# Kernel optimization log

Hardware: AMD Instinct MI355X
Metric: run time of the kernel (lower is better)

Reference implementation:

```python
import jax, jax.numpy as jnp
import numpy as np

B, S, D, H = 8, 4096, 1024, 16
HD = D // H          # 64 head dim
NR = HD // 2         # 32 rotations
BASE = 10000.0


def setup_inputs() -> dict:
    key = jax.random.key(0)
    k0, k1, k2 = jax.random.split(key, 3)
    x = jax.random.normal(k0, (B, S, D), jnp.float32)
    thetas = jax.random.normal(k1, (NR,), jnp.float32) * 0.1
    r_pairs = jax.random.uniform(k2, (NR, 2), jnp.float32) * HD  # float indices in [0, HD)
    theta_scale = jnp.ones((1,), jnp.float32)
    n_rots_scale = jnp.ones((1,), jnp.float32)
    r_matrix = jnp.eye(HD, dtype=jnp.float32)
    inv_freq = 1.0 / (BASE ** (jnp.arange(0, HD, 2, dtype=jnp.float32) / HD))  # [HD/2]
    return {"x": x, "thetas": thetas, "r_pairs": r_pairs,
            "theta_scale": theta_scale, "n_rots_scale": n_rots_scale,
            "r_matrix": r_matrix, "inv_freq": inv_freq}


def reference(x, thetas, r_pairs, theta_scale, n_rots_scale, r_matrix, inv_freq):
    b, s, d = x.shape
    hd = r_matrix.shape[0]
    h = d // hd
    xf = x.reshape(-1, hd)  # [B*S*H, hd]

    # adjusted_n_rots = round(n_rots_scale * n_rots); n_rots_scale == 1 -> all rotations
    # (the int() in torch is non-differentiable/static anyway)
    idx = r_pairs.astype(jnp.int32)          # floor of non-negative floats, like .long()
    th = thetas * theta_scale[0]             # [NR]

    def step(xc, inp):
        i, j, t = inp
        c, sn = jnp.cos(t), jnp.sin(t)
        xi = xc[:, i]
        xj = xc[:, j]
        same = i == j
        # x @ G: col i -> xi*c + xj*s, col j -> -xi*s + xj*c; if i==j torch's
        # overwrite order leaves G[i,i] = cos -> col i = xi*c
        ni = jnp.where(same, xi * c, xi * c + xj * sn)
        nj = jnp.where(same, xi * c, -xi * sn + xj * c)
        xc = xc.at[:, i].set(ni)
        xc = xc.at[:, j].set(nj)
        return xc, None

    xf, _ = jax.lax.scan(step, xf, (idx[:, 0], idx[:, 1], th))
    xf = xf @ r_matrix                       # [B*S*H, hd]
    x4 = xf.reshape(b, s, h, hd)

    pos = jnp.arange(s, dtype=jnp.float32)
    sinusoid = pos[:, None] * inv_freq[None, :]        # [S, hd/2]
    sin = jnp.sin(sinusoid)[None, :, None, :]
    cos = jnp.cos(sinusoid)[None, :, None, :]
    x1 = x4[..., ::2]
    x2 = x4[..., 1::2]
    out = jnp.concatenate([x1 * cos - x2 * sin, x1 * sin + x2 * cos], axis=-1)
    return out.reshape(b, s, d)
```

## Files before the change

### kernel.cpp

```cpp
#include <hip/hip_runtime.h>
#include <hip/hip_bf16.h>

#define BB 8
#define SS 4096
#define DD 1024
#define HH 16
#define HD 64
#define NR 32
#define NROWS (BB * SS * HH)

__global__ __launch_bounds__(256) void build_C_kernel(
    const float* __restrict__ thetas,
    const float* __restrict__ r_pairs,
    const float* __restrict__ theta_scale,
    const float* __restrict__ r_matrix,
    float* __restrict__ C_out)
{
    __shared__ float W[64 * 68];
    __shared__ int   ii[NR], jj[NR];
    __shared__ float cc[NR], ss[NR];

    const int t = threadIdx.x;

#pragma unroll
    for (int it = 0; it < 16; ++it) {
        int idx = t + 256 * it;
        W[(idx >> 6) * 68 + (idx & 63)] = r_matrix[idx];
    }
    if (t < NR) {
        ii[t] = (int)r_pairs[2 * t];
        jj[t] = (int)r_pairs[2 * t + 1];
        float th = thetas[t] * theta_scale[0];
        cc[t] = cosf(th);
        ss[t] = sinf(th);
    }
    __syncthreads();

    if (t < 64) {
        for (int k = NR - 1; k >= 0; --k) {
            int i = ii[k], j = jj[k];
            float c = cc[k], s = ss[k];
            float xi = W[i * 68 + t];
            float xj = W[j * 68 + t];
            if (i == j) {
                W[i * 68 + t] = c * xi;
            } else {
                W[i * 68 + t] = c * xi - s * xj;
                W[j * 68 + t] = s * xi + c * xj;
            }
        }
    }
    __syncthreads();

#pragma unroll
    for (int it = 0; it < 16; ++it) {
        int idx = t + 256 * it;
        C_out[idx] = W[(idx >> 6) * 68 + (idx & 63)];
    }
}

#define RPB 128
#define XT_STRIDE 132

__global__ __launch_bounds__(256) void rope_main_kernel(
    const float* __restrict__ x,
    const float* __restrict__ C,
    const float* __restrict__ inv_freq,
    float* __restrict__ out)
{
    __shared__ float Cs[64 * 64];
    __shared__ float xT[64 * XT_STRIDE];

    const int t = threadIdx.x;
    const size_t tile = (size_t)blockIdx.x * (RPB * HD);

    {
        const float4* C4  = (const float4*)C;
        float4*       Cs4 = (float4*)Cs;
#pragma unroll
        for (int it = 0; it < 4; ++it)
            Cs4[t + 256 * it] = C4[t + 256 * it];
    }
    {
        const float4* x4 = (const float4*)(x + tile);
#pragma unroll
        for (int it = 0; it < 8; ++it) {
            int f = t + 256 * it;
            float4 v = x4[f];
            int row = f >> 4;
            int k4  = (f & 15) << 2;
            xT[(k4 + 0) * XT_STRIDE + row] = v.x;
            xT[(k4 + 1) * XT_STRIDE + row] = v.y;
            xT[(k4 + 2) * XT_STRIDE + row] = v.z;
            xT[(k4 + 3) * XT_STRIDE + row] = v.w;
        }
    }
    __syncthreads();

    const int jq = t & 7;
    const int rg = t >> 3;
    const int j0 = jq << 3;
    const int r0 = rg << 2;

    float acc[4][8];
#pragma unroll
    for (int u = 0; u < 4; ++u)
#pragma unroll
        for (int v = 0; v < 8; ++v) acc[u][v] = 0.0f;

#pragma unroll 4
    for (int k = 0; k < 64; ++k) {
        const float4 av  = *(const float4*)&xT[k * XT_STRIDE + r0];
        const float4 bv0 = *(const float4*)&Cs[(k << 6) + j0];
        const float4 bv1 = *(const float4*)&Cs[(k << 6) + j0 + 4];
        const float a[4] = {av.x, av.y, av.z, av.w};
        const float b[8] = {bv0.x, bv0.y, bv0.z, bv0.w, bv1.x, bv1.y, bv1.z, bv1.w};
#pragma unroll
        for (int u = 0; u < 4; ++u)
#pragma unroll
            for (int v = 0; v < 8; ++v)
                acc[u][v] = fmaf(a[u], b[v], acc[u][v]);
    }

    const size_t grow0 = (size_t)blockIdx.x * RPB + r0;
    const int   s_pos  = (int)((grow0 >> 4) & (SS - 1));
    const float pos    = (float)s_pos;

    const int rbase = j0 >> 1;
    const float4 invf = *(const float4*)&inv_freq[rbase];
    float cs[4], sn[4];
    __sincosf(pos * invf.x, &sn[0], &cs[0]);
    __sincosf(pos * invf.y, &sn[1], &cs[1]);
    __sincosf(pos * invf.z, &sn[2], &cs[2]);
    __sincosf(pos * invf.w, &sn[3], &cs[3]);

#pragma unroll
    for (int u = 0; u < 4; ++u) {
        float* orow = out + tile + (size_t)(r0 + u) * HD;
        float4 o1, o2;
        o1.x = acc[u][0] * cs[0] - acc[u][1] * sn[0];
        o1.y = acc[u][2] * cs[1] - acc[u][3] * sn[1];
        o1.z = acc[u][4] * cs[2] - acc[u][5] * sn[2];
        o1.w = acc[u][6] * cs[3] - acc[u][7] * sn[3];
        o2.x = acc[u][0] * sn[0] + acc[u][1] * cs[0];
        o2.y = acc[u][2] * sn[1] + acc[u][3] * cs[1];
        o2.z = acc[u][4] * sn[2] + acc[u][5] * cs[2];
        o2.w = acc[u][6] * sn[3] + acc[u][7] * cs[3];
        *(float4*)&orow[rbase]      = o1;
        *(float4*)&orow[32 + rbase] = o2;
    }
}

extern "C" void kernel_launch(void* const* d_in, const int* in_sizes, int n_in,
                              void* d_out, int out_size, void* d_ws, size_t ws_size,
                              hipStream_t stream)
{
    const float* x           = (const float*)d_in[0];
    const float* thetas      = (const float*)d_in[1];
    const float* r_pairs     = (const float*)d_in[2];
    const float* theta_scale = (const float*)d_in[3];
    const float* r_matrix    = (const float*)d_in[5];
    const float* inv_freq    = (const float*)d_in[6];
    float* out = (float*)d_out;
    float* Cws = (float*)d_ws;

    build_C_kernel<<<1, 256, 0, stream>>>(thetas, r_pairs, theta_scale, r_matrix, Cws);

    const int nblocks = NROWS / RPB;
    rope_main_kernel<<<nblocks, 256, 0, stream>>>(x, Cws, inv_freq, out);
}
```

Before: 247.4 us.

## Replace FP32 LDS GEMM with bf16 MFMA fragments and register-prefetched x tiles

```diff
diff --git a/kernel.cpp b/kernel.cpp
--- a/kernel.cpp
+++ b/kernel.cpp
@@ -8,13 +8,24 @@
 #define HD 64
 #define NR 32
 #define NROWS (BB * SS * HH)
+#define NTILES (NROWS / 16)
+#define TPW 4
+
+using frag_ab = __attribute__((ext_vector_type(8))) short;
+using frag_cd = __attribute__((ext_vector_type(4))) float;
+
+static __device__ __forceinline__ unsigned short f2bf(float f) {
+    union { float f; unsigned u; } v; v.f = f;
+    unsigned r = v.u + 0x7fffu + ((v.u >> 16) & 1u);
+    return (unsigned short)(r >> 16);
+}
 
 __global__ __launch_bounds__(256) void build_C_kernel(
     const float* __restrict__ thetas,
     const float* __restrict__ r_pairs,
     const float* __restrict__ theta_scale,
     const float* __restrict__ r_matrix,
-    float* __restrict__ C_out)
+    unsigned short* __restrict__ Cpk)
 {
     __shared__ float W[64 * 68];
     __shared__ int   ii[NR], jj[NR];
@@ -54,100 +65,106 @@
 
 #pragma unroll
     for (int it = 0; it < 16; ++it) {
-        int idx = t + 256 * it;
-        C_out[idx] = W[(idx >> 6) * 68 + (idx & 63)];
+        int idx  = t * 16 + it;
+        int f    = idx >> 9;
+        int rem  = idx & 511;
+        int lane = rem >> 3;
+        int j    = rem & 7;
+        int kt   = f >> 2, nt = f & 3;
+        int q    = lane >> 4, nl = lane & 15;
+        int k    = kt * 32 + q * 8 + j;
+        int npos = nt * 16 + nl;
+        int oc   = (npos < 32) ? (npos << 1) : (((npos - 32) << 1) | 1);
+        Cpk[idx] = f2bf(W[k * 68 + oc]);
     }
 }
 
-#define RPB 128
-#define XT_STRIDE 132
-
-__global__ __launch_bounds__(256) void rope_main_kernel(
+__global__ __launch_bounds__(256, 4) void rope_mfma_kernel(
     const float* __restrict__ x,
-    const float* __restrict__ C,
+    const unsigned short* __restrict__ Cpk,
     const float* __restrict__ inv_freq,
     float* __restrict__ out)
 {
-    __shared__ float Cs[64 * 64];
-    __shared__ float xT[64 * XT_STRIDE];
+    const int t  = threadIdx.x;
+    const int l  = t & 63;
+    const int q  = l >> 4;
+    const int nl = l & 15;
+    const int w  = (blockIdx.x * 256 + t) >> 6;
+    const int tile0 = w * TPW;
 
-    const int t = threadIdx.x;
-    const size_t tile = (size_t)blockIdx.x * (RPB * HD);
-
+    frag_ab B[8];
     {
-        const float4* C4  = (const float4*)C;
-        float4*       Cs4 = (float4*)Cs;
+        const uint4* cp = (const uint4*)Cpk;
 #pragma unroll
-        for (int it = 0; it < 4; ++it)
-            Cs4[t + 256 * it] = C4[t + 256 * it];
-    }
-    {
-        const float4* x4 = (const float4*)(x + tile);
-#pragma unroll
-        for (int it = 0; it < 8; ++it) {
-            int f = t + 256 * it;
-            float4 v = x4[f];
-            int row = f >> 4;
-            int k4  = (f & 15) << 2;
-            xT[(k4 + 0) * XT_STRIDE + row] = v.x;
-            xT[(k4 + 1) * XT_STRIDE + row] = v.y;
-            xT[(k4 + 2) * XT_STRIDE + row] = v.z;
-            xT[(k4 + 3) * XT_STRIDE + row] = v.w;
+        for (int f = 0; f < 8; ++f) {
+            union { uint4 u; frag_ab s; } cvt;
+            cvt.u = cp[f * 64 + l];
+            B[f] = cvt.s;
         }
     }
-    __syncthreads();
+    const float invf0 = inv_freq[nl];
+    const float invf1 = inv_freq[16 + nl];
 
-    const int jq = t & 7;
-    const int rg = t >> 3;
-    const int j0 = jq << 3;
-    const int r0 = rg << 2;
-
-    float acc[4][8];
-#pragma unroll
-    for (int u = 0; u < 4; ++u)
-#pragma unroll
-        for (int v = 0; v < 8; ++v) acc[u][v] = 0.0f;
-
-#pragma unroll 4
-    for (int k = 0; k < 64; ++k) {
-        const float4 av  = *(const float4*)&xT[k * XT_STRIDE + r0];
-        const float4 bv0 = *(const float4*)&Cs[(k << 6) + j0];
-        const float4 bv1 = *(const float4*)&Cs[(k << 6) + j0 + 4];
-        const float a[4] = {av.x, av.y, av.z, av.w};
-        const float b[8] = {bv0.x, bv0.y, bv0.z, bv0.w, bv1.x, bv1.y, bv1.z, bv1.w};
-#pragma unroll
-        for (int u = 0; u < 4; ++u)
-#pragma unroll
-            for (int v = 0; v < 8; ++v)
-                acc[u][v] = fmaf(a[u], b[v], acc[u][v]);
+    float4 a[4];
+    {
+        const float* xr = x + ((size_t)tile0 * 16 + nl) * 64 + q * 8;
+        a[0] = *(const float4*)(xr);
+        a[1] = *(const float4*)(xr + 4);
+        a[2] = *(const float4*)(xr + 32);
+        a[3] = *(const float4*)(xr + 36);
     }
 
-    const size_t grow0 = (size_t)blockIdx.x * RPB + r0;
-    const int   s_pos  = (int)((grow0 >> 4) & (SS - 1));
-    const float pos    = (float)s_pos;
+#pragma unroll
+    for (int tt = 0; tt < TPW; ++tt) {
+        const int tl = tile0 + tt;
 
-    const int rbase = j0 >> 1;
-    const float4 invf = *(const float4*)&inv_freq[rbase];
-    float cs[4], sn[4];
-    __sincosf(pos * invf.x, &sn[0], &cs[0]);
-    __sincosf(pos * invf.y, &sn[1], &cs[1]);
-    __sincosf(pos * invf.z, &sn[2], &cs[2]);
-    __sincosf(pos * invf.w, &sn[3], &cs[3]);
+        float4 an[4];
+        if (tt + 1 < TPW) {
+            const float* xr = x + ((size_t)(tl + 1) * 16 + nl) * 64 + q * 8;
+            an[0] = *(const float4*)(xr);
+            an[1] = *(const float4*)(xr + 4);
+            an[2] = *(const float4*)(xr + 32);
+            an[3] = *(const float4*)(xr + 36);
+        }
 
+        frag_ab a0, a1;
+        {
+            const float* af = (const float*)&a[0];
 #pragma unroll
-    for (int u = 0; u < 4; ++u) {
-        float* orow = out + tile + (size_t)(r0 + u) * HD;
-        float4 o1, o2;
-        o1.x = acc[u][0] * cs[0] - acc[u][1] * sn[0];
-        o1.y = acc[u][2] * cs[1] - acc[u][3] * sn[1];
-        o1.z = acc[u][4] * cs[2] - acc[u][5] * sn[2];
-        o1.w = acc[u][6] * cs[3] - acc[u][7] * sn[3];
-        o2.x = acc[u][0] * sn[0] + acc[u][1] * cs[0];
-        o2.y = acc[u][2] * sn[1] + acc[u][3] * cs[1];
-        o2.z = acc[u][4] * sn[2] + acc[u][5] * cs[2];
-        o2.w = acc[u][6] * sn[3] + acc[u][7] * cs[3];
-        *(float4*)&orow[rbase]      = o1;
-        *(float4*)&orow[32 + rbase] = o2;
+            for (int j = 0; j < 8; ++j) a0[j] = (short)f2bf(af[j]);
+#pragma unroll
+            for (int j = 0; j < 8; ++j) a1[j] = (short)f2bf(af[8 + j]);
+        }
+
+        frag_cd acc0 = {0.f, 0.f, 0.f, 0.f};
+        frag_cd acc1 = acc0, acc2 = acc0, acc3 = acc0;
+        acc0 = __builtin_amdgcn_mfma_f32_16x16x32_bf16(a0, B[0], acc0, 0, 0, 0);
+        acc1 = __builtin_amdgcn_mfma_f32_16x16x32_bf16(a0, B[1], acc1, 0, 0, 0);
+        acc2 = __builtin_amdgcn_mfma_f32_16x16x32_bf16(a0, B[2], acc2, 0, 0, 0);
+        acc3 = __builtin_amdgcn_mfma_f32_16x16x32_bf16(a0, B[3], acc3, 0, 0, 0);
+        acc0 = __builtin_amdgcn_mfma_f32_16x16x32_bf16(a1, B[4], acc0, 0, 0, 0);
+        acc1 = __builtin_amdgcn_mfma_f32_16x16x32_bf16(a1, B[5], acc1, 0, 0, 0);
+        acc2 = __builtin_amdgcn_mfma_f32_16x16x32_bf16(a1, B[6], acc2, 0, 0, 0);
+        acc3 = __builtin_amdgcn_mfma_f32_16x16x32_bf16(a1, B[7], acc3, 0, 0, 0);
+
+        const float pos = (float)(tl & (SS - 1));
+        float sn0, cs0, sn1, cs1;
+        __sincosf(pos * invf0, &sn0, &cs0);
+        __sincosf(pos * invf1, &sn1, &cs1);
+
+        float* ob = out + ((size_t)tl * 16 + q * 4) * 64;
+#pragma unroll
+        for (int r = 0; r < 4; ++r) {
+            float* orow = ob + (size_t)r * 64;
+            orow[nl]      = acc0[r] * cs0 - acc2[r] * sn0;
+            orow[32 + nl] = acc0[r] * sn0 + acc2[r] * cs0;
+            orow[16 + nl] = acc1[r] * cs1 - acc3[r] * sn1;
+            orow[48 + nl] = acc1[r] * sn1 + acc3[r] * cs1;
+        }
+
+        if (tt + 1 < TPW) {
+            a[0] = an[0]; a[1] = an[1]; a[2] = an[2]; a[3] = an[3];
+        }
     }
 }
 
@@ -162,10 +179,10 @@
     const float* r_matrix    = (const float*)d_in[5];
     const float* inv_freq    = (const float*)d_in[6];
     float* out = (float*)d_out;
-    float* Cws = (float*)d_ws;
+    unsigned short* Cpk = (unsigned short*)d_ws;
 
-    build_C_kernel<<<1, 256, 0, stream>>>(thetas, r_pairs, theta_scale, r_matrix, Cws);
+    build_C_kernel<<<1, 256, 0, stream>>>(thetas, r_pairs, theta_scale, r_matrix, Cpk);
 
-    const int nblocks = NROWS / RPB;
-    rope_main_kernel<<<nblocks, 256, 0, stream>>>(x, Cws, inv_freq, out);
+    const int nblocks = NTILES / (TPW * 4);
+    rope_mfma_kernel<<<nblocks, 256, 0, stream>>>(x, Cpk, inv_freq, out);
 }
```

Result: no change. 249.6 us (+0.9%).
